# Performance work log

Hardware: AMD Instinct MI355X
Metric: run time of the kernel (lower is better)

## Reference

```python
import jax, jax.numpy as jnp
import numpy as np

N, IN_DIM, OUT_DIM, HEADS = 8192, 256, 64, 2

def setup_inputs() -> dict:
    key = jax.random.key(0)
    k1, k2, k3, k4, k5 = jax.random.split(key, 5)
    x = jax.random.normal(k1, (N, IN_DIM), dtype=jnp.float32)
    adj = jax.random.randint(k2, (N, N), 0, 2, dtype=jnp.int32)
    # nn.Linear(in_dim, out_dim*heads, bias=False): weight [out_dim*heads, in_dim]
    W = jax.random.normal(k3, (OUT_DIM * HEADS, IN_DIM), dtype=jnp.float32) / np.sqrt(IN_DIM)
    attn_l = jax.random.normal(k4, (HEADS, OUT_DIM), dtype=jnp.float32)
    attn_r = jax.random.normal(k5, (HEADS, OUT_DIM), dtype=jnp.float32)
    return {"x": x, "adj": adj, "W": W, "attn_l": attn_l, "attn_r": attn_r}

def reference(x, adj, W, attn_l, attn_r):
    n = x.shape[0]
    h = (x @ W.T).reshape(n, HEADS, OUT_DIM)          # [N, H, D]
    el = jnp.einsum('nhd,hd->nh', h, attn_l)           # [N, H]
    er = jnp.einsum('nhd,hd->nh', h, attn_r)           # [N, H]
    e = el[:, None, :] + er[None, :, :]                # [N, N, H]
    e = jnp.where(adj[:, :, None] == 0, -jnp.inf, e)
    a = jax.nn.softmax(e, axis=1)                      # softmax over source nodes j
    out = jnp.einsum('ijh,jhd->ihd', a, h)             # [N, H, D]
    return out.reshape(n, HEADS * OUT_DIM)
```

## Files before the change

kernel.cpp:

```cpp
#include <hip/hip_runtime.h>
#include <cstdint>
#include <cstddef>

#define N_NODES 8192
#define IN_DIM  256
#define OUT_DIM 64
#define HEADS   2
#define FEAT    128
#define NTILES  9
#define ACC_STRIDE 132
#define KSPLIT  8

typedef __bf16 bf16x8 __attribute__((ext_vector_type(8)));
typedef float  f32x4  __attribute__((ext_vector_type(4)));
typedef int    i32x4  __attribute__((ext_vector_type(4)));
typedef unsigned uu32x4 __attribute__((ext_vector_type(4)));

static __device__ __forceinline__ unsigned short f2bf(float f) {
  unsigned u = __float_as_uint(f);
  u += 0x7FFFu + ((u >> 16) & 1u);
  return (unsigned short)(u >> 16);
}

__global__ __launch_bounds__(256) void k_prep(const float* __restrict__ x,
                                              const float* __restrict__ W,
                                              const float* __restrict__ attn_r,
                                              uint4* __restrict__ frag) {
  const int kb = blockIdx.x;
  const int tid = threadIdx.x;
  const int tx = tid & 15, ty = tid >> 4;
  const int j0 = kb * 32;

  __shared__ float xs[32][68];
  __shared__ float wl[128][68];
  __shared__ unsigned short pk[32][146];

  float acc[2][8] = {};

  for (int kc = 0; kc < IN_DIM; kc += 64) {
    __syncthreads();
#pragma unroll
    for (int p = 0; p < 2; p++) {
      const int slot = p*256 + tid;
      const int r = slot >> 4, k4 = slot & 15;
      *(float4*)&xs[r][k4*4] = *(const float4*)(x + (size_t)(j0 + r)*IN_DIM + kc + k4*4);
    }
#pragma unroll
    for (int p = 0; p < 8; p++) {
      const int slot = p*256 + tid;
      const int r = slot >> 4, k4 = slot & 15;
      *(float4*)&wl[r][k4*4] = *(const float4*)(W + (size_t)r*IN_DIM + kc + k4*4);
    }
    __syncthreads();
#pragma unroll
    for (int k4 = 0; k4 < 16; k4++) {
      float4 xr[2], wr[8];
#pragma unroll
      for (int i = 0; i < 2; i++) xr[i] = *(const float4*)&xs[ty + i*16][k4*4];
#pragma unroll
      for (int jj = 0; jj < 8; jj++) wr[jj] = *(const float4*)&wl[tx + jj*16][k4*4];
#pragma unroll
      for (int i = 0; i < 2; i++)
#pragma unroll
        for (int jj = 0; jj < 8; jj++)
          acc[i][jj] += xr[i].x*wr[jj].x + xr[i].y*wr[jj].y +
                        xr[i].z*wr[jj].z + xr[i].w*wr[jj].w;
    }
  }

  float ar[8];
#pragma unroll
  for (int jj = 0; jj < 8; jj++)
    ar[jj] = attn_r[((jj >> 2)) * OUT_DIM + ((tx + jj*16) & 63)];
  float e0[2] = {}, e1[2] = {};
#pragma unroll
  for (int i = 0; i < 2; i++) {
#pragma unroll
    for (int jj = 0; jj < 4; jj++) e0[i] += acc[i][jj] * ar[jj];
#pragma unroll
    for (int jj = 4; jj < 8; jj++) e1[i] += acc[i][jj] * ar[jj];
  }
#pragma unroll
  for (int m = 1; m <= 8; m <<= 1) {
#pragma unroll
    for (int i = 0; i < 2; i++) {
      e0[i] += __shfl_xor(e0[i], m);
      e1[i] += __shfl_xor(e1[i], m);
    }
  }
  float w0[2], w1[2];
#pragma unroll
  for (int i = 0; i < 2; i++) { w0[i] = __expf(e0[i]); w1[i] = __expf(e1[i]); }

#pragma unroll
  for (int i = 0; i < 2; i++) {
    const int row = ty + i*16;
#pragma unroll
    for (int jj = 0; jj < 8; jj++)
      pk[row][tx + jj*16] = f2bf((jj < 4 ? w0[i] : w1[i]) * acc[i][jj]);
    pk[row][128 + tx] = (tx == 0) ? f2bf(w0[i]) : (tx == 1) ? f2bf(w1[i]) : 0;
  }
  __syncthreads();

#pragma unroll
  for (int t = 0; t < 3; t++) {
    const int wid = t*256 + tid;
    if (wid < 576) {
      const int l = wid & 63, n = wid >> 6;
      const int col = n*16 + (l & 15), jb = (l >> 4) * 8;
      uint4 o;
      o.x = (unsigned)pk[jb+0][col] | ((unsigned)pk[jb+1][col] << 16);
      o.y = (unsigned)pk[jb+2][col] | ((unsigned)pk[jb+3][col] << 16);
      o.z = (unsigned)pk[jb+4][col] | ((unsigned)pk[jb+5][col] << 16);
      o.w = (unsigned)pk[jb+6][col] | ((unsigned)pk[jb+7][col] << 16);
      frag[((size_t)kb*NTILES + n)*64 + l] = o;
    }
  }
}

__global__ __launch_bounds__(256, 2) void k_main(const int* __restrict__ adj,
                                                 const uint4* __restrict__ fragB,
                                                 float* __restrict__ accum) {
  const int mb = blockIdx.x >> 3;
  const int ks = blockIdx.x & 7;
  const int tid = threadIdx.x;
  const int wave = tid >> 6, lane = tid & 63;
  const int m16 = lane & 15, quad = lane >> 4;

  const int row0 = mb*128 + wave*32 + m16;
  const int* a0 = adj + (size_t)row0*N_NODES + ks*1024 + quad*8;
  const int* a1 = a0 + (size_t)16*N_NODES;
  const uint4* bb = fragB + (size_t)(ks*32)*NTILES*64 + lane;

  f32x4 acc0[NTILES], acc1[NTILES];
#pragma unroll
  for (int n = 0; n < NTILES; n++) {
    acc0[n] = (f32x4){0.f, 0.f, 0.f, 0.f};
    acc1[n] = (f32x4){0.f, 0.f, 0.f, 0.f};
  }

  i32x4  Abuf[2][4];
  uu32x4 Bbuf[2][NTILES];

  auto loadA = [&](int kk, int buf) {
    const i32x4* p0 = (const i32x4*)(a0 + kk*32);
    const i32x4* p1 = (const i32x4*)(a1 + kk*32);
    Abuf[buf][0] = __builtin_nontemporal_load(p0);
    Abuf[buf][1] = __builtin_nontemporal_load(p0 + 1);
    Abuf[buf][2] = __builtin_nontemporal_load(p1);
    Abuf[buf][3] = __builtin_nontemporal_load(p1 + 1);
  };
  auto loadB = [&](int kk, int buf) {
    const uu32x4* b = (const uu32x4*)bb;
#pragma unroll
    for (int t = 0; t < NTILES; t++)
      Bbuf[buf][t] = b[(size_t)(kk*NTILES + t)*64];
  };
  auto conv = [&](const i32x4* A) -> bf16x8 {
    const int* ai = (const int*)A;
    unsigned u0 = (ai[0] ? 0x3F80u : 0u) | (ai[1] ? 0x3F800000u : 0u);
    unsigned u1 = (ai[2] ? 0x3F80u : 0u) | (ai[3] ? 0x3F800000u : 0u);
    unsigned u2 = (ai[4] ? 0x3F80u : 0u) | (ai[5] ? 0x3F800000u : 0u);
    unsigned u3 = (ai[6] ? 0x3F80u : 0u) | (ai[7] ? 0x3F800000u : 0u);
    uu32x4 u = {u0, u1, u2, u3};
    return __builtin_bit_cast(bf16x8, u);
  };
  auto compute = [&](int buf) {
    bf16x8 af0 = conv(&Abuf[buf][0]);
    bf16x8 af1 = conv(&Abuf[buf][2]);
#pragma unroll
    for (int n = 0; n < NTILES; n++) {
      bf16x8 bfr = __builtin_bit_cast(bf16x8, Bbuf[buf][n]);
      acc0[n] = __builtin_amdgcn_mfma_f32_16x16x32_bf16(af0, bfr, acc0[n], 0, 0, 0);
    }
#pragma unroll
    for (int n = 0; n < NTILES; n++) {
      bf16x8 bfr = __builtin_bit_cast(bf16x8, Bbuf[buf][n]);
      acc1[n] = __builtin_amdgcn_mfma_f32_16x16x32_bf16(af1, bfr, acc1[n], 0, 0, 0);
    }
  };

  loadA(0, 0); loadB(0, 0);
  for (int kk = 0; kk < 32; kk += 2) {
    loadA(kk + 1, 1); loadB(kk + 1, 1);
    compute(0);
    const int k2 = (kk + 2 < 32) ? kk + 2 : 31;
    loadA(k2, 0); loadB(k2, 0);
    compute(1);
  }

  const int rb0 = mb*128 + wave*32 + quad*4;
  float* op = accum + (size_t)ks*N_NODES*ACC_STRIDE;
#pragma unroll
  for (int n = 0; n < NTILES; n++) {
    if (n == 8 && m16 >= HEADS) continue;
#pragma unroll
    for (int r = 0; r < 4; r++) {
      op[(size_t)(rb0 + r)*ACC_STRIDE + n*16 + m16]      = acc0[n][r];
      op[(size_t)(rb0 + 16 + r)*ACC_STRIDE + n*16 + m16] = acc1[n][r];
    }
  }
}

__global__ void k_div(const float* __restrict__ acc, float* __restrict__ out) {
  const int i = blockIdx.x, c = threadIdx.x;
  const int h = c >> 6;
  float num = 0.f, den = 0.f;
#pragma unroll
  for (int s = 0; s < KSPLIT; s++) {
    const float* p = acc + ((size_t)s*N_NODES + i)*ACC_STRIDE;
    num += p[c];
    den += p[FEAT + h];
  }
  out[(size_t)i*FEAT + c] = num / den;
}

extern "C" void kernel_launch(void* const* d_in, const int* in_sizes, int n_in,
                              void* d_out, int out_size, void* d_ws, size_t ws_size,
                              hipStream_t stream) {
  const float* x      = (const float*)d_in[0];
  const int*   adj    = (const int*)  d_in[1];
  const float* W      = (const float*)d_in[2];
  const float* attn_r = (const float*)d_in[4];

  char* ws = (char*)d_ws;
  uint4* frag = (uint4*)(ws + 0);
  float* acc  = (float*)(ws + 4194304);
  float* out  = (float*)d_out;

  hipLaunchKernelGGL(k_prep, dim3(256),  dim3(256), 0, stream, x, W, attn_r, frag);
  hipLaunchKernelGGL(k_main, dim3(512),  dim3(256), 0, stream, adj, frag, acc);
  hipLaunchKernelGGL(k_div,  dim3(8192), dim3(128), 0, stream, acc, out);
}
```

Before: 434.2 us.

## Halve rows per wave and K-split count in the adjacency MFMA kernel

The main kernel now gives each wave a single 16-row tile instead of two, and splits the source dimension 4 ways instead of 8. Each block therefore covers 64 rows over a K range twice as long, and the grid size stays the same. The goal is to halve the partial-accumulator writes and the reduction reads in k_div, and to free registers by dropping the second accumulator set. The cost is that each B fragment loaded now feeds one MFMA instead of two, so B-fragment traffic per adjacency element doubles.

Result: slower. 599.2 us (+38.0%).

```diff
diff --git a/kernel.cpp b/kernel.cpp
--- a/kernel.cpp
+++ b/kernel.cpp
@@ -9,7 +9,7 @@
 #define FEAT    128
 #define NTILES  9
 #define ACC_STRIDE 132
-#define KSPLIT  8
+#define KSPLIT  4
 
 typedef __bf16 bf16x8 __attribute__((ext_vector_type(8)));
 typedef float  f32x4  __attribute__((ext_vector_type(4)));
@@ -121,34 +121,27 @@
 __global__ __launch_bounds__(256, 2) void k_main(const int* __restrict__ adj,
                                                  const uint4* __restrict__ fragB,
                                                  float* __restrict__ accum) {
-  const int mb = blockIdx.x >> 3;
-  const int ks = blockIdx.x & 7;
+  const int mb = blockIdx.x >> 2;
+  const int ks = blockIdx.x & 3;
   const int tid = threadIdx.x;
   const int wave = tid >> 6, lane = tid & 63;
   const int m16 = lane & 15, quad = lane >> 4;
 
-  const int row0 = mb*128 + wave*32 + m16;
-  const int* a0 = adj + (size_t)row0*N_NODES + ks*1024 + quad*8;
-  const int* a1 = a0 + (size_t)16*N_NODES;
-  const uint4* bb = fragB + (size_t)(ks*32)*NTILES*64 + lane;
-
-  f32x4 acc0[NTILES], acc1[NTILES];
-#pragma unroll
-  for (int n = 0; n < NTILES; n++) {
-    acc0[n] = (f32x4){0.f, 0.f, 0.f, 0.f};
-    acc1[n] = (f32x4){0.f, 0.f, 0.f, 0.f};
-  }
-
-  i32x4  Abuf[2][4];
+  const int row0 = mb*64 + wave*16 + m16;
+  const int* a0 = adj + (size_t)row0*N_NODES + ks*2048 + quad*8;
+  const uint4* bb = fragB + (size_t)(ks*64)*NTILES*64 + lane;
+
+  f32x4 acc[NTILES];
+#pragma unroll
+  for (int n = 0; n < NTILES; n++) acc[n] = (f32x4){0.f, 0.f, 0.f, 0.f};
+
+  i32x4  Abuf[2][2];
   uu32x4 Bbuf[2][NTILES];
 
   auto loadA = [&](int kk, int buf) {
-    const i32x4* p0 = (const i32x4*)(a0 + kk*32);
-    const i32x4* p1 = (const i32x4*)(a1 + kk*32);
-    Abuf[buf][0] = __builtin_nontemporal_load(p0);
-    Abuf[buf][1] = __builtin_nontemporal_load(p0 + 1);
-    Abuf[buf][2] = __builtin_nontemporal_load(p1);
-    Abuf[buf][3] = __builtin_nontemporal_load(p1 + 1);
+    const i32x4* p = (const i32x4*)(a0 + kk*32);
+    Abuf[buf][0] = __builtin_nontemporal_load(p);
+    Abuf[buf][1] = __builtin_nontemporal_load(p + 1);
   };
   auto loadB = [&](int kk, int buf) {
     const uu32x4* b = (const uu32x4*)bb;
@@ -166,39 +159,31 @@
     return __builtin_bit_cast(bf16x8, u);
   };
   auto compute = [&](int buf) {
-    bf16x8 af0 = conv(&Abuf[buf][0]);
-    bf16x8 af1 = conv(&Abuf[buf][2]);
+    bf16x8 af = conv(&Abuf[buf][0]);
 #pragma unroll
     for (int n = 0; n < NTILES; n++) {
       bf16x8 bfr = __builtin_bit_cast(bf16x8, Bbuf[buf][n]);
-      acc0[n] = __builtin_amdgcn_mfma_f32_16x16x32_bf16(af0, bfr, acc0[n], 0, 0, 0);
-    }
-#pragma unroll
-    for (int n = 0; n < NTILES; n++) {
-      bf16x8 bfr = __builtin_bit_cast(bf16x8, Bbuf[buf][n]);
-      acc1[n] = __builtin_amdgcn_mfma_f32_16x16x32_bf16(af1, bfr, acc1[n], 0, 0, 0);
+      acc[n] = __builtin_amdgcn_mfma_f32_16x16x32_bf16(af, bfr, acc[n], 0, 0, 0);
     }
   };
 
   loadA(0, 0); loadB(0, 0);
-  for (int kk = 0; kk < 32; kk += 2) {
+  for (int kk = 0; kk < 64; kk += 2) {
     loadA(kk + 1, 1); loadB(kk + 1, 1);
     compute(0);
-    const int k2 = (kk + 2 < 32) ? kk + 2 : 31;
+    const int k2 = (kk + 2 < 64) ? kk + 2 : 63;
     loadA(k2, 0); loadB(k2, 0);
     compute(1);
   }
 
-  const int rb0 = mb*128 + wave*32 + quad*4;
+  const int rb0 = mb*64 + wave*16 + quad*4;
   float* op = accum + (size_t)ks*N_NODES*ACC_STRIDE;
 #pragma unroll
   for (int n = 0; n < NTILES; n++) {
     if (n == 8 && m16 >= HEADS) continue;
 #pragma unroll
-    for (int r = 0; r < 4; r++) {
-      op[(size_t)(rb0 + r)*ACC_STRIDE + n*16 + m16]      = acc0[n][r];
-      op[(size_t)(rb0 + 16 + r)*ACC_STRIDE + n*16 + m16] = acc1[n][r];
-    }
+    for (int r = 0; r < 4; r++)
+      op[(size_t)(rb0 + r)*ACC_STRIDE + n*16 + m16] = acc[n][r];
   }
 }
 
```

## Stage adjacency tiles into LDS via async global_load_lds with swizzled layout

Applied to the files above, without the earlier changes.

The main kernel now copies 128x32 int tiles of the adjacency matrix into double-buffered shared memory using direct global-to-LDS loads, with an XOR swizzle to avoid bank conflicts. Each wave then reads its MFMA A fragments from LDS instead of loading them per lane straight from global memory. The goal is fully coalesced row-contiguous reads of the large adjacency stream and freed VGPRs. In exchange it adds a block-wide barrier every k-step, and the B fragments are no longer prefetched a step ahead, which can expose load latency.

Measured after the change: 431.0 us. No clear change (-0.8%).

```diff
diff --git a/kernel.cpp b/kernel.cpp
--- a/kernel.cpp
+++ b/kernel.cpp
@@ -127,10 +127,29 @@
   const int wave = tid >> 6, lane = tid & 63;
   const int m16 = lane & 15, quad = lane >> 4;
 
-  const int row0 = mb*128 + wave*32 + m16;
-  const int* a0 = adj + (size_t)row0*N_NODES + ks*1024 + quad*8;
-  const int* a1 = a0 + (size_t)16*N_NODES;
-  const uint4* bb = fragB + (size_t)(ks*32)*NTILES*64 + lane;
+  __shared__ int tile[2][4096];
+
+  const int lr = lane >> 3;
+  const int lc = ((lane & 7) ^ lr) << 2;
+  const int kb0 = ks * 1024;
+  const int* gbase = adj + (size_t)(mb*128)*N_NODES + kb0 + (size_t)lr*N_NODES + lc;
+
+  auto stage = [&](int buf, int kk) {
+#pragma unroll
+    for (int i = 0; i < 4; ++i) {
+      const int c = wave*4 + i;
+      const int* g = gbase + (size_t)(c*8)*N_NODES + kk*32;
+      __builtin_amdgcn_global_load_lds(
+        (const __attribute__((address_space(1))) void*)g,
+        (__attribute__((address_space(3))) void*)&tile[buf][c*256],
+        16, 0, 0);
+    }
+  };
+
+  const int r0 = wave*32 + m16;
+  const int swz = (r0 & 7) << 4;
+  const int a0off = r0*128 + ((quad*32) ^ swz);
+  const uu32x4* bb = (const uu32x4*)fragB + lane;
 
   f32x4 acc0[NTILES], acc1[NTILES];
 #pragma unroll
@@ -139,54 +158,49 @@
     acc1[n] = (f32x4){0.f, 0.f, 0.f, 0.f};
   }
 
-  i32x4  Abuf[2][4];
-  uu32x4 Bbuf[2][NTILES];
-
-  auto loadA = [&](int kk, int buf) {
-    const i32x4* p0 = (const i32x4*)(a0 + kk*32);
-    const i32x4* p1 = (const i32x4*)(a1 + kk*32);
-    Abuf[buf][0] = __builtin_nontemporal_load(p0);
-    Abuf[buf][1] = __builtin_nontemporal_load(p0 + 1);
-    Abuf[buf][2] = __builtin_nontemporal_load(p1);
-    Abuf[buf][3] = __builtin_nontemporal_load(p1 + 1);
-  };
-  auto loadB = [&](int kk, int buf) {
-    const uu32x4* b = (const uu32x4*)bb;
-#pragma unroll
-    for (int t = 0; t < NTILES; t++)
-      Bbuf[buf][t] = b[(size_t)(kk*NTILES + t)*64];
-  };
-  auto conv = [&](const i32x4* A) -> bf16x8 {
-    const int* ai = (const int*)A;
-    unsigned u0 = (ai[0] ? 0x3F80u : 0u) | (ai[1] ? 0x3F800000u : 0u);
-    unsigned u1 = (ai[2] ? 0x3F80u : 0u) | (ai[3] ? 0x3F800000u : 0u);
-    unsigned u2 = (ai[4] ? 0x3F80u : 0u) | (ai[5] ? 0x3F800000u : 0u);
-    unsigned u3 = (ai[6] ? 0x3F80u : 0u) | (ai[7] ? 0x3F800000u : 0u);
+  auto conv8 = [&](i32x4 lo, i32x4 hi) -> bf16x8 {
+    unsigned u0 = (lo[0] ? 0x3F80u : 0u) | (lo[1] ? 0x3F800000u : 0u);
+    unsigned u1 = (lo[2] ? 0x3F80u : 0u) | (lo[3] ? 0x3F800000u : 0u);
+    unsigned u2 = (hi[0] ? 0x3F80u : 0u) | (hi[1] ? 0x3F800000u : 0u);
+    unsigned u3 = (hi[2] ? 0x3F80u : 0u) | (hi[3] ? 0x3F800000u : 0u);
     uu32x4 u = {u0, u1, u2, u3};
     return __builtin_bit_cast(bf16x8, u);
   };
-  auto compute = [&](int buf) {
-    bf16x8 af0 = conv(&Abuf[buf][0]);
-    bf16x8 af1 = conv(&Abuf[buf][2]);
+
+  stage(0, 0);
+  __syncthreads();
+
+  for (int kk = 0; kk < 32; ++kk) {
+    const int cur = kk & 1;
+    if (kk + 1 < 32) stage(cur ^ 1, kk + 1);
+
+    uu32x4 bv[NTILES];
+    {
+      const uu32x4* bp = bb + (size_t)(ks*32 + kk)*NTILES*64;
+#pragma unroll
+      for (int t = 0; t < NTILES; t++) bv[t] = bp[t*64];
+    }
+
+    const char* tb = (const char*)&tile[cur][0];
+    i32x4 x00 = *(const i32x4*)(tb + a0off);
+    i32x4 x01 = *(const i32x4*)(tb + (a0off ^ 16));
+    i32x4 x10 = *(const i32x4*)(tb + a0off + 2048);
+    i32x4 x11 = *(const i32x4*)(tb + (a0off ^ 16) + 2048);
+
+    bf16x8 af0 = conv8(x00, x01);
+    bf16x8 af1 = conv8(x10, x11);
 #pragma unroll
     for (int n = 0; n < NTILES; n++) {
-      bf16x8 bfr = __builtin_bit_cast(bf16x8, Bbuf[buf][n]);
+      bf16x8 bfr = __builtin_bit_cast(bf16x8, bv[n]);
       acc0[n] = __builtin_amdgcn_mfma_f32_16x16x32_bf16(af0, bfr, acc0[n], 0, 0, 0);
     }
 #pragma unroll
     for (int n = 0; n < NTILES; n++) {
-      bf16x8 bfr = __builtin_bit_cast(bf16x8, Bbuf[buf][n]);
+      bf16x8 bfr = __builtin_bit_cast(bf16x8, bv[n]);
       acc1[n] = __builtin_amdgcn_mfma_f32_16x16x32_bf16(af1, bfr, acc1[n], 0, 0, 0);
     }
-  };
-
-  loadA(0, 0); loadB(0, 0);
-  for (int kk = 0; kk < 32; kk += 2) {
-    loadA(kk + 1, 1); loadB(kk + 1, 1);
-    compute(0);
-    const int k2 = (kk + 2 < 32) ? kk + 2 : 31;
-    loadA(k2, 0); loadB(k2, 0);
-    compute(1);
+
+    __syncthreads();
   }
 
   const int rb0 = mb*128 + wave*32 + quad*4;
```
